# Optimization experiments

Measured on AMD Instinct MI355X. Metric: run time of the kernel, lower is better.

## Reference

```python
import jax, jax.numpy as jnp
import numpy as np

T = 0.07  # temperature
EPS = 1e-12

MEM, DIM = 262144, 128
BS, NPOS, NNEG = 256, 8, 1024


def _l2norm(x):
    # torch F.normalize(p=2, dim=1): x / max(||x||, eps)
    n = jnp.sqrt(jnp.sum(x * x, axis=-1, keepdims=True))
    return x / jnp.maximum(n, EPS)


def setup_inputs() -> dict:
    key = jax.random.key(0)
    k = jax.random.split(key, 7)
    return {
        "video_emb": jax.random.normal(k[0], (BS, DIM), jnp.float32),
        "audio_emb": jax.random.normal(k[1], (BS, DIM), jnp.float32),
        "view1_mem": _l2norm(jax.random.normal(k[2], (MEM, DIM), jnp.float32)),
        "view2_mem": _l2norm(jax.random.normal(k[3], (MEM, DIM), jnp.float32)),
        "y": jax.random.randint(k[4], (BS,), 0, MEM, jnp.int32),
        "pos_idx": jax.random.randint(k[5], (BS, NPOS), 0, MEM, jnp.int32),
        "neg_idx": jax.random.randint(k[6], (BS, NNEG), 0, MEM, jnp.int32),
    }


def reference(video_emb, audio_emb, view1_mem, view2_mem, y, pos_idx, neg_idx):
    # normalize query embeddings (xModal=True, wModal=False path)
    v = _l2norm(video_emb)  # (bs, d)
    a = _l2norm(audio_emb)  # (bs, d)

    # no-grad memory gathers
    v_self = view1_mem[y][:, None, :]   # (bs, 1, d)
    a_self = view2_mem[y][:, None, :]
    v_pos = view1_mem[pos_idx]          # (bs, P, d)
    a_pos = view2_mem[pos_idx]
    v_neg = view1_mem[neg_idx]          # (bs, N, d)
    a_neg = view2_mem[neg_idx]

    # xModal scores: targets dotted with context embedding, scaled by 1/T
    xm_a = jnp.concatenate([a_self, a_pos, a_neg], axis=1)  # (bs, 1+P+N, d)
    xm_v = jnp.concatenate([v_self, v_pos, v_neg], axis=1)
    v2a = jnp.einsum('bkd,bd->bk', xm_a, v) / T  # (bs, 1+P+N)
    a2v = jnp.einsum('bkd,bd->bk', xm_v, a) / T
    return jnp.stack([v2a, a2v], axis=0)  # (2, bs, 1+P+N)
```

## Files before the change

kernel.cpp:

```cpp
#include <hip/hip_runtime.h>

#define MEMN 262144
#define DIM 128
#define BS 256
#define NPOS 8
#define NNEG 1024
#define KTOT (1 + NPOS + NNEG)
#define NCHUNK 8
#define CHUNKK ((KTOT + NCHUNK - 1) / NCHUNK)
#define R 8

__global__ __launch_bounds__(256) void avid_sim_kernel(
    const float* __restrict__ video, const float* __restrict__ audio,
    const float* __restrict__ view1, const float* __restrict__ view2,
    const int* __restrict__ y, const int* __restrict__ pos,
    const int* __restrict__ neg, float* __restrict__ out)
{
    const int bid   = blockIdx.x;
    const int m     = bid / (BS * NCHUNK);
    const int rem   = bid - m * (BS * NCHUNK);
    const int b     = rem / NCHUNK;
    const int chunk = rem - b * NCHUNK;

    const float* q_src = (m == 0) ? (video + b * DIM) : (audio + b * DIM);
    const float* mem   = (m == 0) ? view2 : view1;

    const int k0  = chunk * CHUNKK;
    const int cnt = (KTOT - k0 < CHUNKK) ? (KTOT - k0) : CHUNKK;

    __shared__ int s_idx[CHUNKK];
    if ((int)threadIdx.x < cnt) {
        const int k = k0 + (int)threadIdx.x;
        int idx;
        if (k == 0)          idx = y[b];
        else if (k <= NPOS)  idx = pos[b * NPOS + (k - 1)];
        else                 idx = neg[b * NNEG + (k - 1 - NPOS)];
        s_idx[threadIdx.x] = idx;
    }

    const int g   = threadIdx.x & 15;
    const int grp = threadIdx.x >> 4;

    float4 q0 = *(const float4*)(q_src + g * 8);
    float4 q1 = *(const float4*)(q_src + g * 8 + 4);
    float qq = q0.x*q0.x + q0.y*q0.y + q0.z*q0.z + q0.w*q0.w
             + q1.x*q1.x + q1.y*q1.y + q1.z*q1.z + q1.w*q1.w;
    qq += __shfl_xor(qq, 1);
    qq += __shfl_xor(qq, 2);
    qq += __shfl_xor(qq, 4);
    qq += __shfl_xor(qq, 8);
    const float scale = (1.0f / 0.07f) / fmaxf(sqrtf(qq), 1e-12f);
    q0.x *= scale; q0.y *= scale; q0.z *= scale; q0.w *= scale;
    q1.x *= scale; q1.y *= scale; q1.z *= scale; q1.w *= scale;

    __syncthreads();

    float* outm = out + (size_t)m * BS * KTOT + (size_t)b * KTOT + k0;

    int kloc[R];
    const float* rowp[R];
#pragma unroll
    for (int i = 0; i < R; ++i) {
        int k = grp + i * 16;
        kloc[i] = k;
        int kc = (k < cnt) ? k : (cnt - 1);
        rowp[i] = mem + (size_t)s_idx[kc] * DIM + g * 8;
    }
    float4 r0[R], r1[R];
#pragma unroll
    for (int i = 0; i < R; ++i) {
        r0[i] = *(const float4*)(rowp[i]);
        r1[i] = *(const float4*)(rowp[i] + 4);
    }
#pragma unroll
    for (int i = 0; i < R; ++i) {
        float s = q0.x*r0[i].x + q0.y*r0[i].y + q0.z*r0[i].z + q0.w*r0[i].w
                + q1.x*r1[i].x + q1.y*r1[i].y + q1.z*r1[i].z + q1.w*r1[i].w;
        s += __shfl_xor(s, 1);
        s += __shfl_xor(s, 2);
        s += __shfl_xor(s, 4);
        s += __shfl_xor(s, 8);
        if (g == 0 && kloc[i] < cnt) outm[kloc[i]] = s;
    }
    for (int k = grp + R * 16; k < cnt; k += 16) {
        const float* row = mem + (size_t)s_idx[k] * DIM + g * 8;
        float4 a0 = *(const float4*)(row);
        float4 a1 = *(const float4*)(row + 4);
        float s = q0.x*a0.x + q0.y*a0.y + q0.z*a0.z + q0.w*a0.w
                + q1.x*a1.x + q1.y*a1.y + q1.z*a1.z + q1.w*a1.w;
        s += __shfl_xor(s, 1);
        s += __shfl_xor(s, 2);
        s += __shfl_xor(s, 4);
        s += __shfl_xor(s, 8);
        if (g == 0) outm[k] = s;
    }
}

extern "C" void kernel_launch(void* const* d_in, const int* in_sizes, int n_in,
                              void* d_out, int out_size, void* d_ws, size_t ws_size,
                              hipStream_t stream) {
    const float* video = (const float*)d_in[0];
    const float* audio = (const float*)d_in[1];
    const float* view1 = (const float*)d_in[2];
    const float* view2 = (const float*)d_in[3];
    const int*   y     = (const int*)d_in[4];
    const int*   pos   = (const int*)d_in[5];
    const int*   neg   = (const int*)d_in[6];
    float* out = (float*)d_out;

    dim3 grid(2 * BS * NCHUNK);
    dim3 block(256);
    avid_sim_kernel<<<grid, block, 0, stream>>>(video, audio, view1, view2,
                                                y, pos, neg, out);
}
```

Measured before the change: 44.48 us.

## Drop shared-memory index staging; broadcast gather indices via shuffles with 128-row chunks

Rows per block drop from 130 to a fixed 128, so every row fits in the unrolled 8-per-thread-group loads and the serial tail loop goes away. Each lane of a 16-lane group now loads one index directly and broadcasts it with __shfl, which removes the shared-memory index array and the __syncthreads barrier. The grid grows to 9 chunks per batch row, with a mostly empty last chunk. Bounds checks guard the loads and stores.

```diff
diff --git a/kernel.cpp b/kernel.cpp
--- a/kernel.cpp
+++ b/kernel.cpp
@@ -6,8 +6,8 @@
 #define NPOS 8
 #define NNEG 1024
 #define KTOT (1 + NPOS + NNEG)
-#define NCHUNK 8
-#define CHUNKK ((KTOT + NCHUNK - 1) / NCHUNK)
+#define RPB 128
+#define NCHUNK ((KTOT + RPB - 1) / RPB)
 #define R 8
 
 __global__ __launch_bounds__(256) void avid_sim_kernel(
@@ -23,23 +23,20 @@
     const int chunk = rem - b * NCHUNK;
 
     const float* q_src = (m == 0) ? (video + b * DIM) : (audio + b * DIM);
-    const float* mem   = (m == 0) ? view2 : view1;
-
-    const int k0  = chunk * CHUNKK;
-    const int cnt = (KTOT - k0 < CHUNKK) ? (KTOT - k0) : CHUNKK;
-
-    __shared__ int s_idx[CHUNKK];
-    if ((int)threadIdx.x < cnt) {
-        const int k = k0 + (int)threadIdx.x;
-        int idx;
-        if (k == 0)          idx = y[b];
-        else if (k <= NPOS)  idx = pos[b * NPOS + (k - 1)];
-        else                 idx = neg[b * NNEG + (k - 1 - NPOS)];
-        s_idx[threadIdx.x] = idx;
-    }
+    const float* memt  = (m == 0) ? view2 : view1;
 
     const int g   = threadIdx.x & 15;
     const int grp = threadIdx.x >> 4;
+
+    const int kbase = chunk * RPB + grp;
+    int idx_g = 0;
+    if (g < R) {
+        int kk = kbase + g * 16;
+        if (kk >= KTOT) kk = KTOT - 1;
+        if (kk == 0)          idx_g = y[b];
+        else if (kk <= NPOS)  idx_g = pos[b * NPOS + (kk - 1)];
+        else                  idx_g = neg[b * NNEG + (kk - 1 - NPOS)];
+    }
 
     float4 q0 = *(const float4*)(q_src + g * 8);
     float4 q1 = *(const float4*)(q_src + g * 8 + 4);
@@ -53,46 +50,35 @@
     q0.x *= scale; q0.y *= scale; q0.z *= scale; q0.w *= scale;
     q1.x *= scale; q1.y *= scale; q1.z *= scale; q1.w *= scale;
 
-    __syncthreads();
-
-    float* outm = out + (size_t)m * BS * KTOT + (size_t)b * KTOT + k0;
-
-    int kloc[R];
     const float* rowp[R];
 #pragma unroll
     for (int i = 0; i < R; ++i) {
-        int k = grp + i * 16;
-        kloc[i] = k;
-        int kc = (k < cnt) ? k : (cnt - 1);
-        rowp[i] = mem + (size_t)s_idx[kc] * DIM + g * 8;
+        int idx = __shfl(idx_g, i, 16);
+        rowp[i] = memt + (size_t)idx * DIM + g * 8;
     }
+
+    float* outm = out + (size_t)m * BS * KTOT + (size_t)b * KTOT;
+
     float4 r0[R], r1[R];
 #pragma unroll
     for (int i = 0; i < R; ++i) {
-        r0[i] = *(const float4*)(rowp[i]);
-        r1[i] = *(const float4*)(rowp[i] + 4);
+        if (kbase + i * 16 < KTOT) {
+            r0[i] = *(const float4*)(rowp[i]);
+            r1[i] = *(const float4*)(rowp[i] + 4);
+        }
     }
 #pragma unroll
     for (int i = 0; i < R; ++i) {
-        float s = q0.x*r0[i].x + q0.y*r0[i].y + q0.z*r0[i].z + q0.w*r0[i].w
-                + q1.x*r1[i].x + q1.y*r1[i].y + q1.z*r1[i].z + q1.w*r1[i].w;
-        s += __shfl_xor(s, 1);
-        s += __shfl_xor(s, 2);
-        s += __shfl_xor(s, 4);
-        s += __shfl_xor(s, 8);
-        if (g == 0 && kloc[i] < cnt) outm[kloc[i]] = s;
-    }
-    for (int k = grp + R * 16; k < cnt; k += 16) {
-        const float* row = mem + (size_t)s_idx[k] * DIM + g * 8;
-        float4 a0 = *(const float4*)(row);
-        float4 a1 = *(const float4*)(row + 4);
-        float s = q0.x*a0.x + q0.y*a0.y + q0.z*a0.z + q0.w*a0.w
-                + q1.x*a1.x + q1.y*a1.y + q1.z*a1.z + q1.w*a1.w;
-        s += __shfl_xor(s, 1);
-        s += __shfl_xor(s, 2);
-        s += __shfl_xor(s, 4);
-        s += __shfl_xor(s, 8);
-        if (g == 0) outm[k] = s;
+        const int k = kbase + i * 16;
+        if (k < KTOT) {
+            float s = q0.x*r0[i].x + q0.y*r0[i].y + q0.z*r0[i].z + q0.w*r0[i].w
+                    + q1.x*r1[i].x + q1.y*r1[i].y + q1.z*r1[i].z + q1.w*r1[i].w;
+            s += __shfl_xor(s, 1);
+            s += __shfl_xor(s, 2);
+            s += __shfl_xor(s, 4);
+            s += __shfl_xor(s, 8);
+            if (g == 0) outm[k] = s;
+        }
     }
 }
 
```

Measured after the change: 45.33 us. No clear change (+1.9%).

## Sort gather indices per row and reorder block mapping for locality

Applied to the files above, without the earlier changes.

Adds a pre-pass kernel that bitonic-sorts each batch row's 1033 memory indices, each packed with its original position, and writes them to workspace. The gather kernel then reads rows in sorted index order and scatters results back to their original slots. Block order is also changed so chunks are outermost, putting the video and audio passes for a batch row close together. The aim is better cache locality for the random row gathers. The cost is an extra kernel launch with many barrier-synchronised shared-memory passes, plus scattered output writes.

```diff
diff --git a/kernel.cpp b/kernel.cpp
--- a/kernel.cpp
+++ b/kernel.cpp
@@ -5,38 +5,69 @@
 #define BS 256
 #define NPOS 8
 #define NNEG 1024
-#define KTOT (1 + NPOS + NNEG)
+#define KTOT 1033
+#define SORTN 2048
+#define LSTRIDE 1040
 #define NCHUNK 8
-#define CHUNKK ((KTOT + NCHUNK - 1) / NCHUNK)
+#define CHUNKK 130
 #define R 8
 
-__global__ __launch_bounds__(256) void avid_sim_kernel(
+__global__ __launch_bounds__(256) void sort_kernel(
+    const int* __restrict__ y, const int* __restrict__ pos,
+    const int* __restrict__ neg, unsigned* __restrict__ sorted)
+{
+    const int b = blockIdx.x;
+    __shared__ unsigned s[SORTN];
+
+    for (int k = threadIdx.x; k < SORTN; k += 256) {
+        unsigned v = 0xFFFFFFFFu;
+        if (k < KTOT) {
+            int idx;
+            if (k == 0)          idx = y[b];
+            else if (k <= NPOS)  idx = pos[b * NPOS + (k - 1)];
+            else                 idx = neg[b * NNEG + (k - 1 - NPOS)];
+            v = ((unsigned)idx << 11) | (unsigned)k;
+        }
+        s[k] = v;
+    }
+
+    for (unsigned size = 2; size <= SORTN; size <<= 1) {
+        for (unsigned stride = size >> 1; stride > 0; stride >>= 1) {
+            __syncthreads();
+            for (unsigned t = threadIdx.x; t < SORTN / 2; t += 256) {
+                unsigned i = 2 * t - (t & (stride - 1));
+                unsigned j = i + stride;
+                bool dir = ((i & size) == 0);
+                unsigned a = s[i], c = s[j];
+                if ((a > c) == dir) { s[i] = c; s[j] = a; }
+            }
+        }
+    }
+    __syncthreads();
+    for (int t = threadIdx.x; t < KTOT; t += 256)
+        sorted[(size_t)b * LSTRIDE + t] = s[t];
+}
+
+__global__ __launch_bounds__(256) void gather_kernel(
     const float* __restrict__ video, const float* __restrict__ audio,
     const float* __restrict__ view1, const float* __restrict__ view2,
-    const int* __restrict__ y, const int* __restrict__ pos,
-    const int* __restrict__ neg, float* __restrict__ out)
+    const unsigned* __restrict__ sorted, float* __restrict__ out)
 {
     const int bid   = blockIdx.x;
-    const int m     = bid / (BS * NCHUNK);
-    const int rem   = bid - m * (BS * NCHUNK);
-    const int b     = rem / NCHUNK;
-    const int chunk = rem - b * NCHUNK;
+    const int chunk = bid >> 9;
+    const int r     = bid & 511;
+    const int m     = r >> 8;
+    const int b     = r & 255;
 
     const float* q_src = (m == 0) ? (video + b * DIM) : (audio + b * DIM);
-    const float* mem   = (m == 0) ? view2 : view1;
+    const float* memt  = (m == 0) ? view2 : view1;
 
     const int k0  = chunk * CHUNKK;
     const int cnt = (KTOT - k0 < CHUNKK) ? (KTOT - k0) : CHUNKK;
 
-    __shared__ int s_idx[CHUNKK];
-    if ((int)threadIdx.x < cnt) {
-        const int k = k0 + (int)threadIdx.x;
-        int idx;
-        if (k == 0)          idx = y[b];
-        else if (k <= NPOS)  idx = pos[b * NPOS + (k - 1)];
-        else                 idx = neg[b * NNEG + (k - 1 - NPOS)];
-        s_idx[threadIdx.x] = idx;
-    }
+    __shared__ unsigned s_e[CHUNKK];
+    if ((int)threadIdx.x < cnt)
+        s_e[threadIdx.x] = sorted[(size_t)b * LSTRIDE + k0 + threadIdx.x];
 
     const int g   = threadIdx.x & 15;
     const int grp = threadIdx.x >> 4;
@@ -55,16 +86,16 @@
 
     __syncthreads();
 
-    float* outm = out + (size_t)m * BS * KTOT + (size_t)b * KTOT + k0;
+    float* outm = out + (size_t)m * BS * KTOT + (size_t)b * KTOT;
 
-    int kloc[R];
+    unsigned ent[R];
     const float* rowp[R];
 #pragma unroll
     for (int i = 0; i < R; ++i) {
-        int k = grp + i * 16;
-        kloc[i] = k;
-        int kc = (k < cnt) ? k : (cnt - 1);
-        rowp[i] = mem + (size_t)s_idx[kc] * DIM + g * 8;
+        int kk = grp + i * 16;
+        int kc = (kk < cnt) ? kk : (cnt - 1);
+        ent[i] = s_e[kc];
+        rowp[i] = memt + (size_t)(ent[i] >> 11) * DIM + g * 8;
     }
     float4 r0[R], r1[R];
 #pragma unroll
@@ -80,10 +111,11 @@
         s += __shfl_xor(s, 2);
         s += __shfl_xor(s, 4);
         s += __shfl_xor(s, 8);
-        if (g == 0 && kloc[i] < cnt) outm[kloc[i]] = s;
+        if (g == 0 && grp + i * 16 < cnt) outm[ent[i] & 2047u] = s;
     }
-    for (int k = grp + R * 16; k < cnt; k += 16) {
-        const float* row = mem + (size_t)s_idx[k] * DIM + g * 8;
+    for (int kk = grp + R * 16; kk < cnt; kk += 16) {
+        unsigned e = s_e[kk];
+        const float* row = memt + (size_t)(e >> 11) * DIM + g * 8;
         float4 a0 = *(const float4*)(row);
         float4 a1 = *(const float4*)(row + 4);
         float s = q0.x*a0.x + q0.y*a0.y + q0.z*a0.z + q0.w*a0.w
@@ -92,7 +124,7 @@
         s += __shfl_xor(s, 2);
         s += __shfl_xor(s, 4);
         s += __shfl_xor(s, 8);
-        if (g == 0) outm[k] = s;
+        if (g == 0) outm[e & 2047u] = s;
     }
 }
 
@@ -107,9 +139,9 @@
     const int*   pos   = (const int*)d_in[5];
     const int*   neg   = (const int*)d_in[6];
     float* out = (float*)d_out;
+    unsigned* sorted = (unsigned*)d_ws;
 
-    dim3 grid(2 * BS * NCHUNK);
-    dim3 block(256);
-    avid_sim_kernel<<<grid, block, 0, stream>>>(video, audio, view1, view2,
-                                                y, pos, neg, out);
+    sort_kernel<<<BS, 256, 0, stream>>>(y, pos, neg, sorted);
+    gather_kernel<<<2 * BS * NCHUNK, 256, 0, stream>>>(video, audio, view1, view2,
+                                                       sorted, out);
 }
```

Result: slower. 80.72 us (+81.5%).
